# Kernel tuning notes

Hardware: AMD Instinct MI355X
Metric: run time of the kernel (lower is better)

Reference implementation:

```python
import jax, jax.numpy as jnp
import numpy as np

B, S, D = 4, 2048, 1024
H = 16
HD = D // H


def setup_inputs() -> dict:
    key = jax.random.key(0)
    ks = jax.random.split(key, 5)
    scale = 0.02
    return {
        "x": jax.random.normal(ks[0], (B, S, D), dtype=jnp.float32),
        "wq": jax.random.normal(ks[1], (D, D), dtype=jnp.float32) * scale,
        "wk": jax.random.normal(ks[2], (D, D), dtype=jnp.float32) * scale,
        "wv": jax.random.normal(ks[3], (D, D), dtype=jnp.float32) * scale,
        "wo": jax.random.normal(ks[4], (D, D), dtype=jnp.float32) * scale,
    }


def reference(x, wq, wk, wv, wo):
    b, s, _ = x.shape
    # project and split heads: [b, h, s, hd]
    def proj(w):
        return jnp.einsum('bsd,de->bse', x, w).reshape(b, s, H, HD).transpose(0, 2, 1, 3)
    q, k, v = proj(wq), proj(wk), proj(wv)
    scores = jnp.einsum('bhqd,bhkd->bhqk', q, k)
    causal = jnp.tril(jnp.ones((s, s), dtype=bool))  # True = keep
    scores = jnp.where(causal, scores, -jnp.inf)
    attn = jax.nn.softmax(scores / jnp.sqrt(jnp.float32(HD)), axis=-1)
    ctx = jnp.einsum('bhqk,bhkd->bhqd', attn, v)
    ctx = ctx.transpose(0, 2, 1, 3).reshape(b, s, D)
    return jnp.einsum('bsd,de->bse', ctx, wo)
```

## Files before the change

### kernel.cpp

```cpp
#include <hip/hip_runtime.h>

#define S_LEN 2048
#define D_DIM 1024
#define NH    16
#define HD    64
#define BATCH 4
#define M_ROWS 8192

typedef __attribute__((ext_vector_type(8))) short bf16x8;
typedef __attribute__((ext_vector_type(4))) float f32x4;
typedef __attribute__((ext_vector_type(8))) unsigned short u16x8;

__device__ __forceinline__ unsigned short f2bf(float f) {
    unsigned u = __builtin_bit_cast(unsigned, f);
    u = (u + 0x7fffu + ((u >> 16) & 1u)) >> 16;
    return (unsigned short)u;
}
__device__ __forceinline__ unsigned pack2(float a, float b) {
    unsigned ua = __builtin_bit_cast(unsigned, a);
    unsigned ub = __builtin_bit_cast(unsigned, b);
    return ((ua + 0x8000u) >> 16) | ((ub + 0x8000u) & 0xffff0000u);
}

__device__ __forceinline__ void gload16(const void* g, void* l) {
    __builtin_amdgcn_global_load_lds((const __attribute__((address_space(1))) unsigned*)g,
                                     (__attribute__((address_space(3))) unsigned*)l,
                                     16, 0, 0);
}

template<int N> __device__ __forceinline__ void vmwait() {
    if constexpr (N == 0)      asm volatile("s_waitcnt vmcnt(0)" ::: "memory");
    else if constexpr (N == 3) asm volatile("s_waitcnt vmcnt(3)" ::: "memory");
    else if constexpr (N == 4) asm volatile("s_waitcnt vmcnt(4)" ::: "memory");
    else if constexpr (N == 6) asm volatile("s_waitcnt vmcnt(6)" ::: "memory");
    else if constexpr (N == 8) asm volatile("s_waitcnt vmcnt(8)" ::: "memory");
}

__global__ __launch_bounds__(256) void prep_k(const float* __restrict__ x,
                                              const float* __restrict__ w0, const float* __restrict__ w1,
                                              const float* __restrict__ w2, const float* __restrict__ w3,
                                              unsigned short* __restrict__ xbf,
                                              unsigned short* __restrict__ o0, unsigned short* __restrict__ o1,
                                              unsigned short* __restrict__ o2, unsigned short* __restrict__ o3) {
    __shared__ float sT[64][65];
    const int t = threadIdx.x;
    if (blockIdx.x < 4096) {
        size_t i = (size_t)blockIdx.x * 256 + t;
        const float4* xf = (const float4*)x;
        float4 a = xf[2 * i], b = xf[2 * i + 1];
        u16x8 v;
        v[0] = f2bf(a.x); v[1] = f2bf(a.y); v[2] = f2bf(a.z); v[3] = f2bf(a.w);
        v[4] = f2bf(b.x); v[5] = f2bf(b.y); v[6] = f2bf(b.z); v[7] = f2bf(b.w);
        *(u16x8*)(xbf + i * 8) = v;
        return;
    }
    const int wb = blockIdx.x - 4096;
    const int z = wb >> 8;
    const float* w; unsigned short* o;
    switch (z) {
        case 0: w = w0; o = o0; break;
        case 1: w = w1; o = o1; break;
        case 2: w = w2; o = o2; break;
        default: w = w3; o = o3; break;
    }
    const float sc = (z == 0) ? 0.18033688011112042f : 1.0f;
    const int n0 = (wb & 15) * 64, k0 = ((wb >> 4) & 15) * 64;
    const int r = t >> 4, cq = t & 15;
#pragma unroll
    for (int it = 0; it < 4; ++it) {
        int k = r + it * 16;
        float4 v = *(const float4*)&w[(size_t)(k0 + k) * D_DIM + n0 + cq * 4];
        sT[k][cq * 4 + 0] = v.x; sT[k][cq * 4 + 1] = v.y;
        sT[k][cq * 4 + 2] = v.z; sT[k][cq * 4 + 3] = v.w;
    }
    __syncthreads();
    const int n = t >> 2, ch = t & 3;
    union { unsigned short s[8]; uint4 v; } p0, p1;
#pragma unroll
    for (int j = 0; j < 8; ++j) p0.s[j] = f2bf(sT[ch * 16 + j][n] * sc);
#pragma unroll
    for (int j = 0; j < 8; ++j) p1.s[j] = f2bf(sT[ch * 16 + 8 + j][n] * sc);
    *(uint4*)&o[(size_t)(n0 + n) * D_DIM + k0 + ch * 16]     = p0.v;
    *(uint4*)&o[(size_t)(n0 + n) * D_DIM + k0 + ch * 16 + 8] = p1.v;
}

template<int NFRAG, int NGLD>
__device__ __forceinline__ void gemm_core(const unsigned short* __restrict__ A,
                                          const unsigned short* __restrict__ Bt,
                                          unsigned short* __restrict__ sA,
                                          unsigned short* __restrict__ sB,
                                          int m0, int n0, int t,
                                          f32x4 (&acc)[4][NFRAG])
{
    constexpr int BSLOT = (NGLD - 1) * 4096;
    const int lane = t & 63, wid = t >> 6;
    const int mm = lane & 15, quad = lane >> 4;
    const int wm = wid >> 2, wn = wid & 3;

    const int sr = t >> 2;
    const int sg = (t & 3) ^ ((sr >> 1) & 3);
    const unsigned short* asrc  = A  + (size_t)(m0 + sr) * D_DIM + sg * 8;
    const unsigned short* bsrc0 = Bt + (size_t)(n0 + sr) * D_DIM + sg * 8;
    unsigned short* dA = sA + t * 8;
    unsigned short* dB = sB + t * 8;

    const int al = wm * 64 + mm;
    const int bl = wn * (NFRAG * 16) + mm;
    const int xs = quad ^ ((mm >> 1) & 3);

#pragma unroll
    for (int pt = 0; pt < 3; ++pt) {
        const int ko = pt * 32;
        gload16(asrc + ko, dA + pt * 4096);
#pragma unroll
        for (int p = 0; p < NGLD - 1; ++p)
            gload16(bsrc0 + (size_t)p * 128 * D_DIM + ko, dB + pt * BSLOT + p * 4096);
    }
    vmwait<2 * NGLD>();
    __builtin_amdgcn_s_barrier();

#define GTILE(T_, W_, ST_)                                                                 \
{                                                                                          \
    const unsigned soA_ = (unsigned)((T_) & 3) * 4096u;                                    \
    const unsigned soB_ = (unsigned)((T_) & 3) * (unsigned)BSLOT;                          \
    if (ST_) {                                                                             \
        const int ko_ = ((T_) + 3) * 32;                                                   \
        const unsigned wA_ = (unsigned)(((T_) + 3) & 3) * 4096u;                           \
        const unsigned wB_ = (unsigned)(((T_) + 3) & 3) * (unsigned)BSLOT;                 \
        gload16(asrc + ko_, dA + wA_);                                                     \
        _Pragma("unroll")                                                                  \
        for (int p_ = 0; p_ < NGLD - 1; ++p_)                                              \
            gload16(bsrc0 + (size_t)p_ * 128 * D_DIM + ko_, dB + wB_ + p_ * 4096);         \
    }                                                                                      \
    bf16x8 af_[4], bv_[NFRAG];                                                             \
    _Pragma("unroll")                                                                      \
    for (int nf = 0; nf < NFRAG; ++nf)                                                     \
        bv_[nf] = *(const bf16x8*)&sB[soB_ + (unsigned)(bl + nf * 16) * 32 + xs * 8];      \
    _Pragma("unroll")                                                                      \
    for (int mf = 0; mf < 4; ++mf)                                                         \
        af_[mf] = *(const bf16x8*)&sA[soA_ + (unsigned)(al + mf * 16) * 32 + xs * 8];      \
    asm volatile("s_waitcnt lgkmcnt(0)" ::: "memory");                                     \
    __builtin_amdgcn_s_setprio(1);                                                         \
    _Pragma("unroll")                                                                      \
    for (int mf = 0; mf < 4; ++mf)                                                         \
        _Pragma("unroll")                                                                  \
        for (int nf = 0; nf < NFRAG; ++nf)                                                 \
            acc[mf][nf] = __builtin_amdgcn_mfma_f32_16x16x32_bf16(af_[mf], bv_[nf], acc[mf][nf], 0, 0, 0); \
    __builtin_amdgcn_s_setprio(0);                                                         \
    vmwait<(W_)>();                                                                        \
    __builtin_amdgcn_s_barrier();                                                          \
}

#pragma unroll 4
    for (int T = 0; T < 28; ++T) GTILE(T, 2 * NGLD, true);
    GTILE(28, 2 * NGLD, true);
    GTILE(29, NGLD, false);
    GTILE(30, 0, false);
    GTILE(31, -1, false);
#undef GTILE
}

__global__ __launch_bounds__(512, 2) void gemmqkv_k(const unsigned short* __restrict__ A,
                                                    const unsigned short* __restrict__ Bt,
                                                    unsigned short* __restrict__ qb,
                                                    unsigned short* __restrict__ kb,
                                                    unsigned short* __restrict__ vt)
{
    __shared__ unsigned short sA[4 * 4096];
    __shared__ unsigned short sB[4 * 3 * 4096];
    const int t = threadIdx.x;
    const int bid = blockIdx.x;
    const int wg = (bid & 7) * 64 + (bid >> 3);
    const int mt = wg >> 3, nt = wg & 7;
    const int m0 = mt * 128, n0 = nt * 384;

    f32x4 acc[4][6];
#pragma unroll
    for (int i = 0; i < 4; ++i)
#pragma unroll
        for (int j = 0; j < 6; ++j) acc[i][j] = (f32x4){0.f, 0.f, 0.f, 0.f};

    gemm_core<6, 4>(A, Bt, sA, sB, m0, n0, t, acc);

    const int lane = t & 63, wid = t >> 6;
    const int mm = lane & 15, quad = lane >> 4;
    const int wm = wid >> 2, wn = wid & 3;

#pragma unroll
    for (int nf = 0; nf < 6; ++nf) {
        const int c0 = n0 + wn * 96 + nf * 16;
        const int widx = c0 >> 10, nl0 = c0 & 1023;
        if (widx == 2) {
            const int h = nl0 >> 6, hd = (nl0 & 63) + mm;
#pragma unroll
            for (int mf = 0; mf < 4; ++mf) {
                int rglob = m0 + wm * 64 + mf * 16 + quad * 4;
                int bb = rglob >> 11, ss = rglob & (S_LEN - 1);
                union { unsigned short s[4]; unsigned long long ll; } pk;
#pragma unroll
                for (int r = 0; r < 4; ++r) pk.s[r] = f2bf(acc[mf][nf][r]);
                *(unsigned long long*)&vt[((size_t)(bb * NH + h) * HD + hd) * S_LEN + ss] = pk.ll;
            }
        } else {
            unsigned short* outp = widx ? kb : qb;
#pragma unroll
            for (int mf = 0; mf < 4; ++mf)
#pragma unroll
                for (int r = 0; r < 4; ++r)
                    outp[(size_t)(m0 + wm * 64 + mf * 16 + quad * 4 + r) * D_DIM +
                         nl0 + mm] = f2bf(acc[mf][nf][r]);
        }
    }
}

__global__ __launch_bounds__(512, 2) void gemmo_k(const unsigned short* __restrict__ A,
                                                  const unsigned short* __restrict__ Bt,
                                                  float* __restrict__ C)
{
    __shared__ unsigned short sA[4 * 4096];
    __shared__ unsigned short sB[4 * 2 * 4096];
    const int t = threadIdx.x;
    const int bid = blockIdx.x;
    const int wg = (bid & 7) * 32 + (bid >> 3);
    const int mt = wg >> 2, nt = wg & 3;
    const int m0 = mt * 128, n0 = nt * 256;

    f32x4 acc[4][4];
#pragma unroll
    for (int i = 0; i < 4; ++i)
#pragma unroll
        for (int j = 0; j < 4; ++j) acc[i][j] = (f32x4){0.f, 0.f, 0.f, 0.f};

    gemm_core<4, 3>(A, Bt, sA, sB, m0, n0, t, acc);

    const int lane = t & 63, wid = t >> 6;
    const int mm = lane & 15, quad = lane >> 4;
    const int wm = wid >> 2, wn = wid & 3;

#pragma unroll
    for (int mf = 0; mf < 4; ++mf)
#pragma unroll
        for (int nf = 0; nf < 4; ++nf)
#pragma unroll
            for (int r = 0; r < 4; ++r)
                C[(size_t)(m0 + wm * 64 + mf * 16 + quad * 4 + r) * D_DIM +
                  n0 + wn * 64 + nf * 16 + mm] = acc[mf][nf][r];
}

__global__ __launch_bounds__(512, 4) void attn_k(const unsigned short* __restrict__ Q,
                                                 const unsigned short* __restrict__ K,
                                                 const unsigned short* __restrict__ Vt,
                                                 unsigned short* __restrict__ ctx)
{
    __shared__ unsigned short sK [2][64 * 64];
    __shared__ unsigned short sVT[2][64 * 64];
    __shared__ unsigned short sP [128 * 64];
    const int t = threadIdx.x;
    const int lane = t & 63, w = t >> 6;
    const int mm = lane & 15, quad = lane >> 4;
    const int pair = blockIdx.x, bh = blockIdx.y;
    const int b = bh >> 4, hh = bh & 15;
    const size_t rowbase = (size_t)b * S_LEN;
    const int coff = hh * HD;
    const unsigned short* Vh = Vt + (size_t)bh * HD * S_LEN;

    const int sc_ = t >> 3, sj = t & 7;
    const int sgk = sj ^ (sc_ & 7);

    u16x8 onesu;
#pragma unroll
    for (int j = 0; j < 8; ++j) onesu[j] = 0x3F80;
    const bf16x8 ones = __builtin_bit_cast(bf16x8, onesu);

    for (int sidx = 0; sidx < 2; ++sidx) {
        const int qt = sidx ? (15 - pair) : pair;
        const int q0 = qt * 128;

        bf16x8 qf[2];
#pragma unroll
        for (int kk = 0; kk < 2; ++kk)
            qf[kk] = *(const bf16x8*)(Q + (rowbase + q0 + w * 16 + mm) * D_DIM
                                        + coff + kk * 32 + quad * 8);
        f32x4 o[4], lacc;
        lacc = (f32x4){0.f, 0.f, 0.f, 0.f};
#pragma unroll
        for (int hf = 0; hf < 4; ++hf) o[hf] = (f32x4){0.f, 0.f, 0.f, 0.f};

        const int nkt = 2 * qt + 2;
        const int qr = q0 + w * 16 + mm;
        const int qrmax = q0 + w * 16 + 15;
        const int m = w * 16 + mm;

        gload16(K  + (rowbase + sc_) * D_DIM + coff + sgk * 8, (void*)&sK[0][t * 8]);
        gload16(Vh + (size_t)sc_ * S_LEN + sgk * 8,            (void*)&sVT[0][t * 8]);

        for (int kt = 0; kt < nkt; ++kt) {
            const int buf = kt & 1;
            __syncthreads();
            if (kt + 1 < nkt) {
                const int k1 = (kt + 1) * 64;
                gload16(K  + (rowbase + k1 + sc_) * D_DIM + coff + sgk * 8,
                        (void*)&sK[1 - buf][t * 8]);
                gload16(Vh + (size_t)sc_ * S_LEN + k1 + sgk * 8,
                        (void*)&sVT[1 - buf][t * 8]);
            }
            const int k0 = kt * 64;
            if (k0 > qrmax) continue;

            f32x4 sacc[4];
#pragma unroll
            for (int kf = 0; kf < 4; ++kf) sacc[kf] = (f32x4){0.f, 0.f, 0.f, 0.f};
#pragma unroll
            for (int kk = 0; kk < 2; ++kk) {
                bf16x8 ak[4];
#pragma unroll
                for (int kf = 0; kf < 4; ++kf) {
                    int key = kf * 16 + mm;
                    int slot = (kk * 4 + quad) ^ (key & 7);
                    ak[kf] = *(const bf16x8*)&sK[buf][key * 64 + slot * 8];
                }
#pragma unroll
                for (int kf = 0; kf < 4; ++kf)
                    sacc[kf] = __builtin_amdgcn_mfma_f32_16x16x32_bf16(ak[kf], qf[kk], sacc[kf], 0, 0, 0);
            }

            const bool needmask = (k0 + 63) > (q0 + w * 16);
#pragma unroll
            for (int kf = 0; kf < 4; ++kf) {
                float p[4];
#pragma unroll
                for (int r = 0; r < 4; ++r) {
                    p[r] = __builtin_amdgcn_exp2f(sacc[kf][r]);
                    if (needmask && (k0 + kf * 16 + quad * 4 + r) > qr) p[r] = 0.f;
                }
                unsigned lo = pack2(p[0], p[1]), hi = pack2(p[2], p[3]);
                int slot = (kf * 2 + (quad >> 1)) ^ (m & 7);
                *(unsigned long long*)&sP[m * 64 + slot * 8 + (quad & 1) * 4] =
                    ((unsigned long long)hi << 32) | lo;
            }

#pragma unroll
            for (int kk = 0; kk < 2; ++kk) {
                bf16x8 pf, vf[4];
                {
                    int slot = (kk * 4 + quad) ^ (m & 7);
                    pf = *(const bf16x8*)&sP[m * 64 + slot * 8];
                }
#pragma unroll
                for (int hf = 0; hf < 4; ++hf) {
                    int hd = hf * 16 + mm;
                    int slot = (kk * 4 + quad) ^ (hd & 7);
                    vf[hf] = *(const bf16x8*)&sVT[buf][hd * 64 + slot * 8];
                }
                lacc = __builtin_amdgcn_mfma_f32_16x16x32_bf16(pf, ones, lacc, 0, 0, 0);
#pragma unroll
                for (int hf = 0; hf < 4; ++hf)
                    o[hf] = __builtin_amdgcn_mfma_f32_16x16x32_bf16(pf, vf[hf], o[hf], 0, 0, 0);
            }
        }
        __syncthreads();

#pragma unroll
        for (int r = 0; r < 4; ++r) {
            float inv = 1.f / lacc[r];
            int row = q0 + w * 16 + quad * 4 + r;
#pragma unroll
            for (int hf = 0; hf < 4; ++hf)
                ctx[(rowbase + row) * D_DIM + coff + hf * 16 + mm] = f2bf(o[hf][r] * inv);
        }
    }
}

extern "C" void kernel_launch(void* const* d_in, const int* in_sizes, int n_in,
                              void* d_out, int out_size, void* d_ws, size_t ws_size,
                              hipStream_t stream)
{
    const float* x  = (const float*)d_in[0];
    const float* wq = (const float*)d_in[1];
    const float* wk = (const float*)d_in[2];
    const float* wv = (const float*)d_in[3];
    const float* wo = (const float*)d_in[4];

    const size_t XE = (size_t)M_ROWS * D_DIM;
    const size_t WE = (size_t)D_DIM * D_DIM;
    unsigned short* ws  = (unsigned short*)d_ws;
    unsigned short* xbf = ws;
    unsigned short* wt0 = xbf + XE;
    unsigned short* wt1 = wt0 + WE;
    unsigned short* wt2 = wt1 + WE;
    unsigned short* wt3 = wt2 + WE;
    unsigned short* qb  = wt3 + WE;
    unsigned short* kb  = qb + XE;
    unsigned short* vt  = kb + XE;
    unsigned short* cb  = vt + XE;

    prep_k<<<dim3(4096 + 1024), 256, 0, stream>>>(x, wq, wk, wv, wo,
                                                  xbf, wt0, wt1, wt2, wt3);

    gemmqkv_k<<<dim3(512), 512, 0, stream>>>(xbf, wt0, qb, kb, vt);

    attn_k<<<dim3(8, BATCH * NH), 512, 0, stream>>>(qb, kb, vt, cb);

    gemmo_k<<<dim3(256), 512, 0, stream>>>(cb, wt3, (float*)d_out);
}
```

Measured before the change: 252.3 us.

## Enlarge QKV GEMM tile to 256x384 and restructure pipeline into 3-stage phased loop

The QKV projection GEMM now uses 256-row tiles (8 M-fragments per wave) with half as many workgroups, raising operand reuse per LDS load. The shared gemm_core moves from a 4-slot, 3-ahead prefetch to a 3-slot ring buffer with 2-ahead prefetch. Each k-step is split into phases that interleave global-to-LDS loads with MFMA pairs, with barriers between phases. The larger accumulator raises register pressure and the grid now has only 256 blocks, and the extra barriers may add sync cost.

```diff
diff --git a/kernel.cpp b/kernel.cpp
--- a/kernel.cpp
+++ b/kernel.cpp
@@ -31,9 +31,7 @@
 template<int N> __device__ __forceinline__ void vmwait() {
     if constexpr (N == 0)      asm volatile("s_waitcnt vmcnt(0)" ::: "memory");
     else if constexpr (N == 3) asm volatile("s_waitcnt vmcnt(3)" ::: "memory");
-    else if constexpr (N == 4) asm volatile("s_waitcnt vmcnt(4)" ::: "memory");
-    else if constexpr (N == 6) asm volatile("s_waitcnt vmcnt(6)" ::: "memory");
-    else if constexpr (N == 8) asm volatile("s_waitcnt vmcnt(8)" ::: "memory");
+    else if constexpr (N == 5) asm volatile("s_waitcnt vmcnt(5)" ::: "memory");
 }
 
 __global__ __launch_bounds__(256) void prep_k(const float* __restrict__ x,
@@ -84,80 +82,97 @@
     *(uint4*)&o[(size_t)(n0 + n) * D_DIM + k0 + ch * 16 + 8] = p1.v;
 }
 
-template<int NFRAG, int NGLD>
+template<int MFRAG, int NFRAG, int AGLD, int BGLD>
 __device__ __forceinline__ void gemm_core(const unsigned short* __restrict__ A,
                                           const unsigned short* __restrict__ Bt,
                                           unsigned short* __restrict__ sA,
                                           unsigned short* __restrict__ sB,
                                           int m0, int n0, int t,
-                                          f32x4 (&acc)[4][NFRAG])
+                                          f32x4 (&acc)[MFRAG][NFRAG])
 {
-    constexpr int BSLOT = (NGLD - 1) * 4096;
+    constexpr int NGLD  = AGLD + BGLD;
+    constexpr int ASLOT = AGLD * 4096;
+    constexpr int BSLOT = BGLD * 4096;
+    constexpr int NPH   = MFRAG / 2;
+
     const int lane = t & 63, wid = t >> 6;
     const int mm = lane & 15, quad = lane >> 4;
     const int wm = wid >> 2, wn = wid & 3;
 
     const int sr = t >> 2;
     const int sg = (t & 3) ^ ((sr >> 1) & 3);
-    const unsigned short* asrc  = A  + (size_t)(m0 + sr) * D_DIM + sg * 8;
-    const unsigned short* bsrc0 = Bt + (size_t)(n0 + sr) * D_DIM + sg * 8;
+    const unsigned short* asrc = A  + (size_t)(m0 + sr) * D_DIM + sg * 8;
+    const unsigned short* bsrc = Bt + (size_t)(n0 + sr) * D_DIM + sg * 8;
     unsigned short* dA = sA + t * 8;
     unsigned short* dB = sB + t * 8;
 
-    const int al = wm * 64 + mm;
+    const int al = wm * (MFRAG * 16) + mm;
     const int bl = wn * (NFRAG * 16) + mm;
     const int xs = quad ^ ((mm >> 1) & 3);
 
 #pragma unroll
-    for (int pt = 0; pt < 3; ++pt) {
+    for (int pt = 0; pt < 2; ++pt) {
         const int ko = pt * 32;
-        gload16(asrc + ko, dA + pt * 4096);
-#pragma unroll
-        for (int p = 0; p < NGLD - 1; ++p)
-            gload16(bsrc0 + (size_t)p * 128 * D_DIM + ko, dB + pt * BSLOT + p * 4096);
-    }
-    vmwait<2 * NGLD>();
+#pragma unroll
+        for (int i = 0; i < AGLD; ++i)
+            gload16(asrc + (size_t)i * 128 * D_DIM + ko, dA + pt * ASLOT + i * 4096);
+#pragma unroll
+        for (int i = 0; i < BGLD; ++i)
+            gload16(bsrc + (size_t)i * 128 * D_DIM + ko, dB + pt * BSLOT + i * 4096);
+    }
+    vmwait<NGLD>();
     __builtin_amdgcn_s_barrier();
 
-#define GTILE(T_, W_, ST_)                                                                 \
-{                                                                                          \
-    const unsigned soA_ = (unsigned)((T_) & 3) * 4096u;                                    \
-    const unsigned soB_ = (unsigned)((T_) & 3) * (unsigned)BSLOT;                          \
-    if (ST_) {                                                                             \
-        const int ko_ = ((T_) + 3) * 32;                                                   \
-        const unsigned wA_ = (unsigned)(((T_) + 3) & 3) * 4096u;                           \
-        const unsigned wB_ = (unsigned)(((T_) + 3) & 3) * (unsigned)BSLOT;                 \
-        gload16(asrc + ko_, dA + wA_);                                                     \
-        _Pragma("unroll")                                                                  \
-        for (int p_ = 0; p_ < NGLD - 1; ++p_)                                              \
-            gload16(bsrc0 + (size_t)p_ * 128 * D_DIM + ko_, dB + wB_ + p_ * 4096);         \
-    }                                                                                      \
-    bf16x8 af_[4], bv_[NFRAG];                                                             \
-    _Pragma("unroll")                                                                      \
-    for (int nf = 0; nf < NFRAG; ++nf)                                                     \
-        bv_[nf] = *(const bf16x8*)&sB[soB_ + (unsigned)(bl + nf * 16) * 32 + xs * 8];      \
-    _Pragma("unroll")                                                                      \
-    for (int mf = 0; mf < 4; ++mf)                                                         \
-        af_[mf] = *(const bf16x8*)&sA[soA_ + (unsigned)(al + mf * 16) * 32 + xs * 8];      \
-    asm volatile("s_waitcnt lgkmcnt(0)" ::: "memory");                                     \
-    __builtin_amdgcn_s_setprio(1);                                                         \
-    _Pragma("unroll")                                                                      \
-    for (int mf = 0; mf < 4; ++mf)                                                         \
-        _Pragma("unroll")                                                                  \
-        for (int nf = 0; nf < NFRAG; ++nf)                                                 \
-            acc[mf][nf] = __builtin_amdgcn_mfma_f32_16x16x32_bf16(af_[mf], bv_[nf], acc[mf][nf], 0, 0, 0); \
-    __builtin_amdgcn_s_setprio(0);                                                         \
-    vmwait<(W_)>();                                                                        \
-    __builtin_amdgcn_s_barrier();                                                          \
-}
-
-#pragma unroll 4
-    for (int T = 0; T < 28; ++T) GTILE(T, 2 * NGLD, true);
-    GTILE(28, 2 * NGLD, true);
-    GTILE(29, NGLD, false);
-    GTILE(30, 0, false);
-    GTILE(31, -1, false);
-#undef GTILE
+    int sRead = 0, sWrite = 2;
+    for (int T = 0; T < 32; ++T) {
+        const int soA = sRead * ASLOT, soB = sRead * BSLOT;
+        const int woA = sWrite * ASLOT, woB = sWrite * BSLOT;
+        const int ko = (T + 2) * 32;
+        const bool st = (T <= 29);
+
+        bf16x8 bv[NFRAG];
+#pragma unroll
+        for (int p = 0; p < NPH; ++p) {
+            if (p == 0) {
+#pragma unroll
+                for (int nf = 0; nf < NFRAG; ++nf)
+                    bv[nf] = *(const bf16x8*)&sB[soB + (bl + nf * 16) * 32 + xs * 8];
+            }
+            bf16x8 af0 = *(const bf16x8*)&sA[soA + (al + (2 * p) * 16) * 32 + xs * 8];
+            bf16x8 af1 = *(const bf16x8*)&sA[soA + (al + (2 * p + 1) * 16) * 32 + xs * 8];
+
+            if (st) {
+                if (p == 0) {
+#pragma unroll
+                    for (int i = 0; i < AGLD; ++i)
+                        gload16(asrc + (size_t)i * 128 * D_DIM + ko, dA + woA + i * 4096);
+                } else {
+#pragma unroll
+                    for (int i = 0; i < BGLD; ++i)
+                        if ((i % (NPH - 1)) == p - 1)
+                            gload16(bsrc + (size_t)i * 128 * D_DIM + ko, dB + woB + i * 4096);
+                }
+            }
+
+            __builtin_amdgcn_s_barrier();
+            asm volatile("s_waitcnt lgkmcnt(0)" ::: "memory");
+            __builtin_amdgcn_s_setprio(1);
+#pragma unroll
+            for (int nf = 0; nf < NFRAG; ++nf) {
+                acc[2 * p][nf]     = __builtin_amdgcn_mfma_f32_16x16x32_bf16(af0, bv[nf], acc[2 * p][nf], 0, 0, 0);
+                acc[2 * p + 1][nf] = __builtin_amdgcn_mfma_f32_16x16x32_bf16(af1, bv[nf], acc[2 * p + 1][nf], 0, 0, 0);
+            }
+            __builtin_amdgcn_s_setprio(0);
+            if (p == NPH - 1) {
+                if (T <= 29)      vmwait<NGLD>();
+                else if (T == 30) vmwait<0>();
+            }
+            __builtin_amdgcn_s_barrier();
+        }
+
+        sRead  = (sRead  == 2) ? 0 : sRead + 1;
+        sWrite = (sWrite == 2) ? 0 : sWrite + 1;
+    }
 }
 
 __global__ __launch_bounds__(512, 2) void gemmqkv_k(const unsigned short* __restrict__ A,
@@ -166,21 +181,21 @@
                                                     unsigned short* __restrict__ kb,
                                                     unsigned short* __restrict__ vt)
 {
-    __shared__ unsigned short sA[4 * 4096];
-    __shared__ unsigned short sB[4 * 3 * 4096];
+    __shared__ unsigned short sA[3 * 2 * 4096];
+    __shared__ unsigned short sB[3 * 3 * 4096];
     const int t = threadIdx.x;
     const int bid = blockIdx.x;
-    const int wg = (bid & 7) * 64 + (bid >> 3);
+    const int wg = (bid & 7) * 32 + (bid >> 3);
     const int mt = wg >> 3, nt = wg & 7;
-    const int m0 = mt * 128, n0 = nt * 384;
-
-    f32x4 acc[4][6];
-#pragma unroll
-    for (int i = 0; i < 4; ++i)
+    const int m0 = mt * 256, n0 = nt * 384;
+
+    f32x4 acc[8][6];
+#pragma unroll
+    for (int i = 0; i < 8; ++i)
 #pragma unroll
         for (int j = 0; j < 6; ++j) acc[i][j] = (f32x4){0.f, 0.f, 0.f, 0.f};
 
-    gemm_core<6, 4>(A, Bt, sA, sB, m0, n0, t, acc);
+    gemm_core<8, 6, 2, 3>(A, Bt, sA, sB, m0, n0, t, acc);
 
     const int lane = t & 63, wid = t >> 6;
     const int mm = lane & 15, quad = lane >> 4;
@@ -193,8 +208,8 @@
         if (widx == 2) {
             const int h = nl0 >> 6, hd = (nl0 & 63) + mm;
 #pragma unroll
-            for (int mf = 0; mf < 4; ++mf) {
-                int rglob = m0 + wm * 64 + mf * 16 + quad * 4;
+            for (int mf = 0; mf < 8; ++mf) {
+                int rglob = m0 + wm * 128 + mf * 16 + quad * 4;
                 int bb = rglob >> 11, ss = rglob & (S_LEN - 1);
                 union { unsigned short s[4]; unsigned long long ll; } pk;
 #pragma unroll
@@ -204,10 +219,10 @@
         } else {
             unsigned short* outp = widx ? kb : qb;
 #pragma unroll
-            for (int mf = 0; mf < 4; ++mf)
+            for (int mf = 0; mf < 8; ++mf)
 #pragma unroll
                 for (int r = 0; r < 4; ++r)
-                    outp[(size_t)(m0 + wm * 64 + mf * 16 + quad * 4 + r) * D_DIM +
+                    outp[(size_t)(m0 + wm * 128 + mf * 16 + quad * 4 + r) * D_DIM +
                          nl0 + mm] = f2bf(acc[mf][nf][r]);
         }
     }
@@ -217,8 +232,8 @@
                                                   const unsigned short* __restrict__ Bt,
                                                   float* __restrict__ C)
 {
-    __shared__ unsigned short sA[4 * 4096];
-    __shared__ unsigned short sB[4 * 2 * 4096];
+    __shared__ unsigned short sA[3 * 4096];
+    __shared__ unsigned short sB[3 * 2 * 4096];
     const int t = threadIdx.x;
     const int bid = blockIdx.x;
     const int wg = (bid & 7) * 32 + (bid >> 3);
@@ -231,7 +246,7 @@
 #pragma unroll
         for (int j = 0; j < 4; ++j) acc[i][j] = (f32x4){0.f, 0.f, 0.f, 0.f};
 
-    gemm_core<4, 3>(A, Bt, sA, sB, m0, n0, t, acc);
+    gemm_core<4, 4, 1, 2>(A, Bt, sA, sB, m0, n0, t, acc);
 
     const int lane = t & 63, wid = t >> 6;
     const int mm = lane & 15, quad = lane >> 4;
@@ -397,7 +412,7 @@
     prep_k<<<dim3(4096 + 1024), 256, 0, stream>>>(x, wq, wk, wv, wo,
                                                   xbf, wt0, wt1, wt2, wt3);
 
-    gemmqkv_k<<<dim3(512), 512, 0, stream>>>(xbf, wt0, qb, kb, vt);
+    gemmqkv_k<<<dim3(256), 512, 0, stream>>>(xbf, wt0, qb, kb, vt);
 
     attn_k<<<dim3(8, BATCH * NH), 512, 0, stream>>>(qb, kb, vt, cb);
 
```

Measured after the change: 244.0 us. -3.3%, faster.
